# Kernel optimization log

Measured on AMD Instinct MI355X. Metric: run time of the kernel, lower is better.

The kernel has to match this reference:

```python
import jax, jax.numpy as jnp
import numpy as np

B, N, F_IN, D = 4, 2048, 32, 64  # D = output_dim; gat1: heads=4, d=D//2=32; gat2: heads=1, d=D


def _gat(x, adj_norm, Wq, bq, Wk, bk, Wv, bv, heads, d):
    b, n, _ = x.shape
    q = (x @ Wq + bq).reshape(b, n, heads, d)
    k = (x @ Wk + bk).reshape(b, n, heads, d)
    v = (x @ Wv + bv).reshape(b, n, heads, d)
    scores = jnp.einsum('bihd,bjhd->bhij', q, k) / jnp.sqrt(jnp.float32(d))
    mask = jnp.where(adj_norm == 0, jnp.float32(-1e9), jnp.float32(0.0))  # [N,N]
    w = jax.nn.softmax(scores + mask[None, None], axis=-1)
    out = jnp.einsum('bhij,bjhd->bihd', w, v)
    return out.reshape(b, n, heads * d)


def setup_inputs() -> dict:
    key = jax.random.key(0)
    ks = jax.random.split(key, 12)
    s = 0.05
    x = jax.random.normal(ks[0], (B, N, F_IN), dtype=jnp.float32)
    adj = (jax.random.uniform(ks[1], (N, N)) < 0.02).astype(jnp.float32)  # sparse binary graph
    return {
        'x': x, 'adj': adj,
        'Wp': jax.random.normal(ks[2], (F_IN, D)) * s, 'bp': jnp.zeros((D,), jnp.float32),
        'Wq1': jax.random.normal(ks[3], (F_IN, 2 * D)) * s, 'bq1': jnp.zeros((2 * D,), jnp.float32),
        'Wk1': jax.random.normal(ks[4], (F_IN, 2 * D)) * s, 'bk1': jnp.zeros((2 * D,), jnp.float32),
        'Wv1': jax.random.normal(ks[5], (F_IN, 2 * D)) * s, 'bv1': jnp.zeros((2 * D,), jnp.float32),
        'Wq2': jax.random.normal(ks[6], (2 * D, D)) * s, 'bq2': jnp.zeros((D,), jnp.float32),
        'Wk2': jax.random.normal(ks[7], (2 * D, D)) * s, 'bk2': jnp.zeros((D,), jnp.float32),
        'Wv2': jax.random.normal(ks[8], (2 * D, D)) * s, 'bv2': jnp.zeros((D,), jnp.float32),
        'gamma': jnp.ones((D,), jnp.float32), 'beta': jnp.zeros((D,), jnp.float32),
    }


def reference(x, adj, Wp, bp, Wq1, bq1, Wk1, bk1, Wv1, bv1,
              Wq2, bq2, Wk2, bk2, Wv2, bv2, gamma, beta):
    # row-normalized adjacency (normalize_adjacency)
    adj_n = adj / (jnp.sum(adj, axis=1, keepdims=True) + 1e-6)
    proj = x @ Wp + bp                                   # [B,N,D]
    h = _gat(x, adj_n, Wq1, bq1, Wk1, bk1, Wv1, bv1, 4, D // 2)   # [B,N,2D]
    h = jax.nn.relu(h)                                   # dropout inactive (training=False)
    h = _gat(h, adj_n, Wq2, bq2, Wk2, bk2, Wv2, bv2, 1, D)        # [B,N,D]
    y = h + proj
    mu = jnp.mean(y, axis=-1, keepdims=True)
    var = jnp.var(y, axis=-1, keepdims=True)
    return gamma * (y - mu) / jnp.sqrt(var + 1e-6) + beta
```

## Files before the change

### kernel.cpp

```cpp
#include <hip/hip_runtime.h>
#include <hip/hip_bf16.h>
#include <hip/hip_fp16.h>

#define BB 4
#define NN 2048
#define FIN 32
#define DD 64
#define MAXDEG 128

__device__ __forceinline__ __half2 u2h2(unsigned u) {
    union { unsigned u; __half2 h; } x; x.u = u; return x.h;
}

__global__ __launch_bounds__(128) void csr_gemm1(const float* __restrict__ adj,
    int* __restrict__ deg, int* __restrict__ col,
    const float* __restrict__ x,
    const float* __restrict__ Wp, const float* __restrict__ bp,
    const float* __restrict__ Wq, const float* __restrict__ bq,
    const float* __restrict__ Wk, const float* __restrict__ bk,
    const float* __restrict__ Wv, const float* __restrict__ bv,
    float* __restrict__ proj, __half* __restrict__ q1,
    __half* __restrict__ k1, __half* __restrict__ v1) {
    const int bid = blockIdx.x;
    const int tid = threadIdx.x;

    if (bid < NN / 2) {
        const int lane = tid & 63;
        const int i = bid * 2 + (tid >> 6);
        const unsigned long long below = (1ull << lane) - 1ull;
        int base = 0;
        for (int j0 = 0; j0 < NN; j0 += 256) {
            const float4 a = *(const float4*)(adj + (size_t)i * NN + j0 + lane * 4);
            const bool n0 = a.x != 0.0f, n1 = a.y != 0.0f, n2 = a.z != 0.0f, n3 = a.w != 0.0f;
            const unsigned long long m0 = __ballot(n0);
            const unsigned long long m1 = __ballot(n1);
            const unsigned long long m2 = __ballot(n2);
            const unsigned long long m3 = __ballot(n3);
            int slot = base + __popcll(m0 & below) + __popcll(m1 & below)
                            + __popcll(m2 & below) + __popcll(m3 & below);
            const int jb = j0 + 4 * lane;
            if (n0) { if (slot < MAXDEG) col[i * MAXDEG + slot] = jb;     ++slot; }
            if (n1) { if (slot < MAXDEG) col[i * MAXDEG + slot] = jb + 1; ++slot; }
            if (n2) { if (slot < MAXDEG) col[i * MAXDEG + slot] = jb + 2; ++slot; }
            if (n3) { if (slot < MAXDEG) col[i * MAXDEG + slot] = jb + 3; ++slot; }
            base += __popcll(m0) + __popcll(m1) + __popcll(m2) + __popcll(m3);
        }
        if (lane == 0) deg[i] = base < MAXDEG ? base : MAXDEG;
        return;
    }

    const int g = bid - NN / 2;
    const int b = g & 3;
    const int half = (g >> 2) & 1;
    const int w = g >> 3;
    const int r0 = b * NN + half * 1024 + w * 4;
    __shared__ float xs[FIN * 4];
    {
        const int r = tid >> 5, k = tid & 31;
        xs[k * 4 + r] = x[(size_t)r0 * FIN + tid];
    }
    __syncthreads();

    float aq0 = bq[tid], aq1 = aq0, aq2 = aq0, aq3 = aq0;
    float ak0 = bk[tid], ak1 = ak0, ak2 = ak0, ak3 = ak0;
    float av0 = bv[tid], av1 = av0, av2 = av0, av3 = av0;
    #pragma unroll
    for (int k = 0; k < FIN; ++k) {
        const float wq = Wq[k * 128 + tid];
        const float wk = Wk[k * 128 + tid];
        const float wv = Wv[k * 128 + tid];
        const float4 xv = *(const float4*)&xs[k * 4];
        aq0 = fmaf(xv.x, wq, aq0); aq1 = fmaf(xv.y, wq, aq1);
        aq2 = fmaf(xv.z, wq, aq2); aq3 = fmaf(xv.w, wq, aq3);
        ak0 = fmaf(xv.x, wk, ak0); ak1 = fmaf(xv.y, wk, ak1);
        ak2 = fmaf(xv.z, wk, ak2); ak3 = fmaf(xv.w, wk, ak3);
        av0 = fmaf(xv.x, wv, av0); av1 = fmaf(xv.y, wv, av1);
        av2 = fmaf(xv.z, wv, av2); av3 = fmaf(xv.w, wv, av3);
    }
    q1[(size_t)(r0 + 0) * 128 + tid] = __float2half_rn(aq0);
    q1[(size_t)(r0 + 1) * 128 + tid] = __float2half_rn(aq1);
    q1[(size_t)(r0 + 2) * 128 + tid] = __float2half_rn(aq2);
    q1[(size_t)(r0 + 3) * 128 + tid] = __float2half_rn(aq3);
    k1[(size_t)(r0 + 0) * 128 + tid] = __float2half_rn(ak0);
    k1[(size_t)(r0 + 1) * 128 + tid] = __float2half_rn(ak1);
    k1[(size_t)(r0 + 2) * 128 + tid] = __float2half_rn(ak2);
    k1[(size_t)(r0 + 3) * 128 + tid] = __float2half_rn(ak3);
    v1[(size_t)(r0 + 0) * 128 + tid] = __float2half_rn(av0);
    v1[(size_t)(r0 + 1) * 128 + tid] = __float2half_rn(av1);
    v1[(size_t)(r0 + 2) * 128 + tid] = __float2half_rn(av2);
    v1[(size_t)(r0 + 3) * 128 + tid] = __float2half_rn(av3);

    if (tid < 64) {
        float a0 = bp[tid], a1 = a0, a2 = a0, a3 = a0;
        #pragma unroll
        for (int k = 0; k < FIN; ++k) {
            const float wp = Wp[k * 64 + tid];
            const float4 xv = *(const float4*)&xs[k * 4];
            a0 = fmaf(xv.x, wp, a0); a1 = fmaf(xv.y, wp, a1);
            a2 = fmaf(xv.z, wp, a2); a3 = fmaf(xv.w, wp, a3);
        }
        proj[(size_t)(r0 + 0) * 64 + tid] = a0; proj[(size_t)(r0 + 1) * 64 + tid] = a1;
        proj[(size_t)(r0 + 2) * 64 + tid] = a2; proj[(size_t)(r0 + 3) * 64 + tid] = a3;
    }
}

__global__ __launch_bounds__(192) void gemm2_fused(const __half* __restrict__ h,
    const float* __restrict__ Wq, const float* __restrict__ bq,
    const float* __restrict__ Wk, const float* __restrict__ bk,
    const float* __restrict__ Wv, const float* __restrict__ bv,
    __half* __restrict__ q2, __half* __restrict__ k2, __half* __restrict__ v2) {
    const int bid = blockIdx.x;
    const int b = bid & 3;
    const int half = (bid >> 2) & 1;
    const int w = bid >> 3;
    const int r0 = b * NN + half * 1024 + w * 8;
    const int tid = threadIdx.x;
    const int mat = tid / 64;
    const int c = tid & 63;
    __shared__ float xs[128][8];
    for (int idx = tid; idx < 512; idx += 192) {
        const __half2 hv = ((const __half2*)(h + (size_t)r0 * 128))[idx];
        const int flat = idx * 2;
        const int r = flat >> 7, k = flat & 127;
        xs[k][r] = __low2float(hv); xs[k + 1][r] = __high2float(hv);
    }
    __syncthreads();

    const float* __restrict__ W   = mat == 0 ? Wq : (mat == 1 ? Wk : Wv);
    const float* __restrict__ bia = mat == 0 ? bq : (mat == 1 ? bk : bv);
    __half* __restrict__ Y        = mat == 0 ? q2 : (mat == 1 ? k2 : v2);

    float acc[8];
    const float b0 = bia[c];
    #pragma unroll
    for (int r = 0; r < 8; ++r) acc[r] = b0;
    #pragma unroll 4
    for (int k = 0; k < 128; ++k) {
        const float wv = W[(size_t)k * 64 + c];
        const float4 xa = *(const float4*)&xs[k][0];
        const float4 xb = *(const float4*)&xs[k][4];
        acc[0] = fmaf(xa.x, wv, acc[0]); acc[1] = fmaf(xa.y, wv, acc[1]);
        acc[2] = fmaf(xa.z, wv, acc[2]); acc[3] = fmaf(xa.w, wv, acc[3]);
        acc[4] = fmaf(xb.x, wv, acc[4]); acc[5] = fmaf(xb.y, wv, acc[5]);
        acc[6] = fmaf(xb.z, wv, acc[6]); acc[7] = fmaf(xb.w, wv, acc[7]);
    }
    #pragma unroll
    for (int r = 0; r < 8; ++r) Y[(size_t)(r0 + r) * 64 + c] = __float2half_rn(acc[r]);
}

__device__ __forceinline__ void map_bi4(int bid, int wid, int& b, int& i) {
    const int xcd = bid & 7;
    b = xcd & 3;
    i = ((xcd >> 2) << 10) | ((bid >> 3) << 2) | wid;
}

__global__ __launch_bounds__(256) void attn1_relu(const __half* __restrict__ q1,
                                                  const __half* __restrict__ k1,
                                                  const __half* __restrict__ v1,
                                                  const int* __restrict__ deg,
                                                  const int* __restrict__ col,
                                                  __half* __restrict__ h) {
    const int wid = threadIdx.x >> 6;
    const int lane = threadIdx.x & 63;
    int b, i;
    map_bi4(blockIdx.x, wid, b, i);

    __shared__ float wsA[4][4][MAXDEG + 8];
    const size_t stride = (size_t)NN * 128;
    const size_t bbase = (size_t)b * stride;
    const int d = deg[i];

    int jA = 0, jB = 0;
    if (lane < d) jA = col[i * MAXDEG + lane];
    if (64 + lane < d) jB = col[i * MAXDEG + 64 + lane];

    const int hh   = lane >> 4;
    const int t    = lane & 15;
    const int nbr8 = t & 7;
    const int e    = t >> 3;

    __half2 qh[8];
    {
        const __half* qbase = q1 + bbase + (size_t)i * 128 + hh * 32 + e * 16;
        const uint4 qa = *(const uint4*)qbase;
        const uint4 qb = *(const uint4*)(qbase + 8);
        qh[0] = u2h2(qa.x); qh[1] = u2h2(qa.y); qh[2] = u2h2(qa.z); qh[3] = u2h2(qa.w);
        qh[4] = u2h2(qb.x); qh[5] = u2h2(qb.y); qh[6] = u2h2(qb.z); qh[7] = u2h2(qb.w);
    }

    const float scale = 0.17677669529663687f;
    float sc[16];
    #pragma unroll
    for (int r = 0; r < 16; ++r) sc[r] = -INFINITY;

    #pragma unroll
    for (int r = 0; r < 16; ++r) {
        if (r * 8 < d) {
            const int slot = r * 8 + nbr8;
            const int jx = __shfl(jA, slot & 63);
            const int jy = __shfl(jB, slot & 63);
            const int j = (slot < 64) ? jx : jy;
            float p = 0.0f;
            if (slot < d) {
                const __half* kr = k1 + bbase + (size_t)j * 128 + hh * 32 + e * 16;
                const uint4 ka = *(const uint4*)kr;
                const uint4 kb = *(const uint4*)(kr + 8);
                __half2 a2 = __float2half2_rn(0.0f), b2 = __float2half2_rn(0.0f);
                a2 = __hfma2(qh[0], u2h2(ka.x), a2); b2 = __hfma2(qh[1], u2h2(ka.y), b2);
                a2 = __hfma2(qh[2], u2h2(ka.z), a2); b2 = __hfma2(qh[3], u2h2(ka.w), b2);
                a2 = __hfma2(qh[4], u2h2(kb.x), a2); b2 = __hfma2(qh[5], u2h2(kb.y), b2);
                a2 = __hfma2(qh[6], u2h2(kb.z), a2); b2 = __hfma2(qh[7], u2h2(kb.w), b2);
                p = (__low2float(a2) + __high2float(a2)) +
                    (__low2float(b2) + __high2float(b2));
            }
            p += __shfl_xor(p, 8);
            if (slot < d) sc[r] = p * scale;
        }
    }

    float mx = -INFINITY;
    #pragma unroll
    for (int r = 0; r < 16; ++r) mx = fmaxf(mx, sc[r]);
    #pragma unroll
    for (int off = 8; off >= 1; off >>= 1) mx = fmaxf(mx, __shfl_xor(mx, off));
    float se = 0.0f;
    #pragma unroll
    for (int r = 0; r < 16; ++r) {
        if (r * 8 < d) {
            const float ex = __expf(sc[r] - mx);
            sc[r] = ex;
            se += ex;
        }
    }
    #pragma unroll
    for (int off = 8; off >= 1; off >>= 1) se += __shfl_xor(se, off);
    const float inv = (d > 0) ? 2.0f / se : 0.0f;
    if (e == 0) {
        #pragma unroll
        for (int r = 0; r < 16; ++r) {
            if (r * 8 < d) {
                const int slot = r * 8 + nbr8;
                if (slot < d) wsA[wid][hh][slot] = sc[r] * inv;
            }
        }
    }
    asm volatile("s_waitcnt lgkmcnt(0)" ::: "memory");

    const float* __restrict__ wp = wsA[wid][lane >> 4];
    const int4* __restrict__ cp4 = (const int4*)(col + i * MAXDEG);
    const __half* __restrict__ vrow = v1 + bbase + 2 * lane;
    float a0 = 0.0f, a1 = 0.0f, b0 = 0.0f, b1 = 0.0f;
    float c0 = 0.0f, c1 = 0.0f, e0 = 0.0f, e1 = 0.0f;
    int t2 = 0;
    for (; t2 + 4 <= d; t2 += 4) {
        const int4 j4 = cp4[t2 >> 2];
        const float w0 = wp[t2], w1 = wp[t2 + 1], w2 = wp[t2 + 2], w3 = wp[t2 + 3];
        const __half2 v0 = u2h2(*(const unsigned*)(vrow + (size_t)j4.x * 128));
        const __half2 v1h = u2h2(*(const unsigned*)(vrow + (size_t)j4.y * 128));
        const __half2 v2h = u2h2(*(const unsigned*)(vrow + (size_t)j4.z * 128));
        const __half2 v3h = u2h2(*(const unsigned*)(vrow + (size_t)j4.w * 128));
        a0 = fmaf(w0, __low2float(v0), a0);  a1 = fmaf(w0, __high2float(v0), a1);
        b0 = fmaf(w1, __low2float(v1h), b0); b1 = fmaf(w1, __high2float(v1h), b1);
        c0 = fmaf(w2, __low2float(v2h), c0); c1 = fmaf(w2, __high2float(v2h), c1);
        e0 = fmaf(w3, __low2float(v3h), e0); e1 = fmaf(w3, __high2float(v3h), e1);
    }
    for (; t2 < d; ++t2) {
        const int j = col[i * MAXDEG + t2];
        const float w0 = wp[t2];
        const __half2 v0 = u2h2(*(const unsigned*)(vrow + (size_t)j * 128));
        a0 = fmaf(w0, __low2float(v0), a0);  a1 = fmaf(w0, __high2float(v0), a1);
    }
    float o0 = (a0 + b0) + (c0 + e0);
    float o1 = (a1 + b1) + (c1 + e1);
    if (d == 0) {
        float s0 = 0.0f, s1 = 0.0f;
        for (int j = 0; j < NN; ++j) {
            const __half2 vj = u2h2(*(const unsigned*)(vrow + (size_t)j * 128));
            s0 += __low2float(vj); s1 += __high2float(vj);
        }
        o0 = s0 * (1.0f / NN); o1 = s1 * (1.0f / NN);
    }
    o0 = fmaxf(o0, 0.0f); o1 = fmaxf(o1, 0.0f);
    ((__half2*)(h + bbase + (size_t)i * 128))[lane] =
        __halves2half2(__float2half_rn(o0), __float2half_rn(o1));
}

__global__ __launch_bounds__(256) void attn2_ln(const __half* __restrict__ q2,
                                                const __half* __restrict__ k2,
                                                const __half* __restrict__ v2,
                                                const float* __restrict__ proj,
                                                const int* __restrict__ deg,
                                                const int* __restrict__ col,
                                                const float* __restrict__ gamma,
                                                const float* __restrict__ beta,
                                                float* __restrict__ out) {
    const int wid = threadIdx.x >> 6;
    const int lane = threadIdx.x & 63;
    int b, i;
    map_bi4(blockIdx.x, wid, b, i);

    __shared__ float ws2[4][MAXDEG];
    __shared__ float att_lds[4][64];
    const size_t stride = (size_t)NN * 64;
    const size_t bbase = (size_t)b * stride;
    const int d = deg[i];

    int jA = 0, jB = 0;
    if (lane < d) jA = col[i * MAXDEG + lane];
    if (64 + lane < d) jB = col[i * MAXDEG + 64 + lane];

    const int g = lane >> 3;
    const int e = lane & 7;

    __half2 qh[4];
    {
        const uint4 qa = *(const uint4*)(q2 + bbase + (size_t)i * 64 + e * 8);
        qh[0] = u2h2(qa.x); qh[1] = u2h2(qa.y); qh[2] = u2h2(qa.z); qh[3] = u2h2(qa.w);
    }

    const float scale = 0.125f;
    float sc[16];
    #pragma unroll
    for (int r = 0; r < 16; ++r) sc[r] = -INFINITY;

    #pragma unroll
    for (int r = 0; r < 16; ++r) {
        if (r * 8 < d) {
            const int slot = r * 8 + g;
            const int jx = __shfl(jA, slot & 63);
            const int jy = __shfl(jB, slot & 63);
            const int j = (slot < 64) ? jx : jy;
            float p = 0.0f;
            if (slot < d) {
                const uint4 ka = *(const uint4*)(k2 + bbase + (size_t)j * 64 + e * 8);
                __half2 a2 = __float2half2_rn(0.0f), b2 = __float2half2_rn(0.0f);
                a2 = __hfma2(qh[0], u2h2(ka.x), a2); b2 = __hfma2(qh[1], u2h2(ka.y), b2);
                a2 = __hfma2(qh[2], u2h2(ka.z), a2); b2 = __hfma2(qh[3], u2h2(ka.w), b2);
                p = (__low2float(a2) + __high2float(a2)) +
                    (__low2float(b2) + __high2float(b2));
            }
            p += __shfl_xor(p, 1);
            p += __shfl_xor(p, 2);
            p += __shfl_xor(p, 4);
            if (slot < d) sc[r] = p * scale;
        }
    }

    float mx = -INFINITY;
    #pragma unroll
    for (int r = 0; r < 16; ++r) mx = fmaxf(mx, sc[r]);
    #pragma unroll
    for (int off = 32; off >= 1; off >>= 1) mx = fmaxf(mx, __shfl_xor(mx, off));
    float se = 0.0f;
    #pragma unroll
    for (int r = 0; r < 16; ++r) {
        if (r * 8 < d) {
            const float ex = __expf(sc[r] - mx);
            sc[r] = ex;
            se += ex;
        }
    }
    #pragma unroll
    for (int off = 32; off >= 1; off >>= 1) se += __shfl_xor(se, off);
    const float inv = (d > 0) ? 8.0f / se : 0.0f;
    if (e == 0) {
        #pragma unroll
        for (int r = 0; r < 16; ++r) {
            if (r * 8 < d) {
                const int slot = r * 8 + g;
                if (slot < d) ws2[wid][slot] = sc[r] * inv;
            }
        }
    }
    asm volatile("s_waitcnt lgkmcnt(0)" ::: "memory");

    const int p = lane & 31, g2 = lane >> 5;
    const float* __restrict__ wp = ws2[wid];
    const __half* __restrict__ vrow = v2 + bbase + 2 * p;
    float a0 = 0.0f, a1 = 0.0f, b0 = 0.0f, b1 = 0.0f;
    int t2 = g2;
    for (; t2 + 2 < d; t2 += 4) {
        const int ja = col[i * MAXDEG + t2], jb = col[i * MAXDEG + t2 + 2];
        const __half2 va = u2h2(*(const unsigned*)(vrow + (size_t)ja * 64));
        const __half2 vb = u2h2(*(const unsigned*)(vrow + (size_t)jb * 64));
        const float wa = wp[t2], wb = wp[t2 + 2];
        a0 = fmaf(wa, __low2float(va), a0); a1 = fmaf(wa, __high2float(va), a1);
        b0 = fmaf(wb, __low2float(vb), b0); b1 = fmaf(wb, __high2float(vb), b1);
    }
    if (t2 < d) {
        const int ja = col[i * MAXDEG + t2];
        const __half2 va = u2h2(*(const unsigned*)(vrow + (size_t)ja * 64));
        const float wa = wp[t2];
        a0 = fmaf(wa, __low2float(va), a0); a1 = fmaf(wa, __high2float(va), a1);
    }
    a0 += b0; a1 += b1;
    a0 += __shfl_xor(a0, 32);
    a1 += __shfl_xor(a1, 32);
    if (g2 == 0) { att_lds[wid][2 * p] = a0; att_lds[wid][2 * p + 1] = a1; }
    asm volatile("s_waitcnt lgkmcnt(0)" ::: "memory");
    float att = att_lds[wid][lane];
    if (d == 0) {
        float a = 0.0f;
        const __half* vr = v2 + bbase + lane;
        for (int j = 0; j < NN; ++j) a += __half2float(vr[(size_t)j * 64]);
        att = a * (1.0f / NN);
    }

    const float y = att + proj[bbase + (size_t)i * 64 + lane];
    float s = y;
    s += __shfl_xor(s, 32); s += __shfl_xor(s, 16); s += __shfl_xor(s, 8);
    s += __shfl_xor(s, 4);  s += __shfl_xor(s, 2);  s += __shfl_xor(s, 1);
    const float mu = s * (1.0f / 64.0f);
    const float yc = y - mu;
    float sq = yc * yc;
    sq += __shfl_xor(sq, 32); sq += __shfl_xor(sq, 16); sq += __shfl_xor(sq, 8);
    sq += __shfl_xor(sq, 4);  sq += __shfl_xor(sq, 2);  sq += __shfl_xor(sq, 1);
    const float var = sq * (1.0f / 64.0f);
    out[bbase + (size_t)i * 64 + lane] =
        gamma[lane] * yc * rsqrtf(var + 1e-6f) + beta[lane];
}

extern "C" void kernel_launch(void* const* d_in, const int* in_sizes, int n_in,
                              void* d_out, int out_size, void* d_ws, size_t ws_size,
                              hipStream_t stream) {
    const float* x     = (const float*)d_in[0];
    const float* adj   = (const float*)d_in[1];
    const float* Wp    = (const float*)d_in[2];
    const float* bp    = (const float*)d_in[3];
    const float* Wq1   = (const float*)d_in[4];
    const float* bq1   = (const float*)d_in[5];
    const float* Wk1   = (const float*)d_in[6];
    const float* bk1   = (const float*)d_in[7];
    const float* Wv1   = (const float*)d_in[8];
    const float* bv1   = (const float*)d_in[9];
    const float* Wq2   = (const float*)d_in[10];
    const float* bq2   = (const float*)d_in[11];
    const float* Wk2   = (const float*)d_in[12];
    const float* bk2   = (const float*)d_in[13];
    const float* Wv2   = (const float*)d_in[14];
    const float* bv2   = (const float*)d_in[15];
    const float* gamma = (const float*)d_in[16];
    const float* beta  = (const float*)d_in[17];
    float* out = (float*)d_out;

    char* ws = (char*)d_ws;
    size_t off = 0;
    auto alloc = [&](size_t bytes) {
        void* p = ws + off;
        off = (off + bytes + 255) & ~(size_t)255;
        return p;
    };
    int*    deg  = (int*)   alloc((size_t)NN * 4);
    int*    col  = (int*)   alloc((size_t)NN * MAXDEG * 4);
    float*  proj = (float*) alloc((size_t)BB * NN * 64 * 4);
    __half* q1   = (__half*)alloc((size_t)BB * NN * 128 * 2);
    __half* k1   = (__half*)alloc((size_t)BB * NN * 128 * 2);
    __half* v1   = (__half*)alloc((size_t)BB * NN * 128 * 2);
    __half* h    = (__half*)alloc((size_t)BB * NN * 128 * 2);
    __half* q2   = (__half*)alloc((size_t)BB * NN * 64 * 2);
    __half* k2   = (__half*)alloc((size_t)BB * NN * 64 * 2);
    __half* v2   = (__half*)alloc((size_t)BB * NN * 64 * 2);

    csr_gemm1<<<NN / 2 + BB * NN / 4, 128, 0, stream>>>(
        adj, deg, col, x, Wp, bp, Wq1, bq1, Wk1, bk1, Wv1, bv1, proj, q1, k1, v1);

    attn1_relu<<<BB * NN / 4, 256, 0, stream>>>(q1, k1, v1, deg, col, h);

    gemm2_fused<<<BB * NN / 8, 192, 0, stream>>>(h, Wq2, bq2, Wk2, bk2, Wv2, bv2,
                                                 q2, k2, v2);

    attn2_ln<<<BB * NN / 4, 256, 0, stream>>>(q2, k2, v2, proj, deg, col, gamma, beta, out);
}
```

Before: 62.95 us.

## Fuse second-layer QKV projection into first attention kernel via shared memory

```diff
diff --git a/kernel.cpp b/kernel.cpp
--- a/kernel.cpp
+++ b/kernel.cpp
@@ -5,22 +5,24 @@
 #define BB 4
 #define NN 2048
 #define FIN 32
-#define DD 64
 #define MAXDEG 128
 
 __device__ __forceinline__ __half2 u2h2(unsigned u) {
     union { unsigned u; __half2 h; } x; x.u = u; return x.h;
 }
 
-__global__ __launch_bounds__(128) void csr_gemm1(const float* __restrict__ adj,
+__global__ __launch_bounds__(128) void csr_gemm1w(const float* __restrict__ adj,
     int* __restrict__ deg, int* __restrict__ col,
     const float* __restrict__ x,
     const float* __restrict__ Wp, const float* __restrict__ bp,
     const float* __restrict__ Wq, const float* __restrict__ bq,
     const float* __restrict__ Wk, const float* __restrict__ bk,
     const float* __restrict__ Wv, const float* __restrict__ bv,
+    const float* __restrict__ Wq2, const float* __restrict__ Wk2,
+    const float* __restrict__ Wv2,
     float* __restrict__ proj, __half* __restrict__ q1,
-    __half* __restrict__ k1, __half* __restrict__ v1) {
+    __half* __restrict__ k1, __half* __restrict__ v1,
+    __half* __restrict__ Wh) {
     const int bid = blockIdx.x;
     const int tid = threadIdx.x;
 
@@ -48,12 +50,17 @@
         if (lane == 0) deg[i] = base < MAXDEG ? base : MAXDEG;
         return;
     }
-
-    const int g = bid - NN / 2;
-    const int b = g & 3;
-    const int half = (g >> 2) & 1;
-    const int w = g >> 3;
-    const int r0 = b * NN + half * 1024 + w * 4;
+    if (bid >= NN / 2 + 2048) {
+        const int t0 = (bid - NN / 2 - 2048) * 128 + tid;
+        for (int e2 = t0; e2 < 3 * 8192; e2 += 256) {
+            const int mat = e2 >> 13, idx = e2 & 8191;
+            const float* src = mat == 0 ? Wq2 : (mat == 1 ? Wk2 : Wv2);
+            Wh[e2] = __float2half_rn(src[idx]);
+        }
+        return;
+    }
+
+    const int r0 = (bid - NN / 2) * 4;
     __shared__ float xs[FIN * 4];
     {
         const int r = tid >> 5, k = tid & 31;
@@ -104,68 +111,26 @@
     }
 }
 
-__global__ __launch_bounds__(192) void gemm2_fused(const __half* __restrict__ h,
-    const float* __restrict__ Wq, const float* __restrict__ bq,
-    const float* __restrict__ Wk, const float* __restrict__ bk,
-    const float* __restrict__ Wv, const float* __restrict__ bv,
-    __half* __restrict__ q2, __half* __restrict__ k2, __half* __restrict__ v2) {
-    const int bid = blockIdx.x;
-    const int b = bid & 3;
-    const int half = (bid >> 2) & 1;
-    const int w = bid >> 3;
-    const int r0 = b * NN + half * 1024 + w * 8;
-    const int tid = threadIdx.x;
-    const int mat = tid / 64;
-    const int c = tid & 63;
-    __shared__ float xs[128][8];
-    for (int idx = tid; idx < 512; idx += 192) {
-        const __half2 hv = ((const __half2*)(h + (size_t)r0 * 128))[idx];
-        const int flat = idx * 2;
-        const int r = flat >> 7, k = flat & 127;
-        xs[k][r] = __low2float(hv); xs[k + 1][r] = __high2float(hv);
-    }
-    __syncthreads();
-
-    const float* __restrict__ W   = mat == 0 ? Wq : (mat == 1 ? Wk : Wv);
-    const float* __restrict__ bia = mat == 0 ? bq : (mat == 1 ? bk : bv);
-    __half* __restrict__ Y        = mat == 0 ? q2 : (mat == 1 ? k2 : v2);
-
-    float acc[8];
-    const float b0 = bia[c];
-    #pragma unroll
-    for (int r = 0; r < 8; ++r) acc[r] = b0;
-    #pragma unroll 4
-    for (int k = 0; k < 128; ++k) {
-        const float wv = W[(size_t)k * 64 + c];
-        const float4 xa = *(const float4*)&xs[k][0];
-        const float4 xb = *(const float4*)&xs[k][4];
-        acc[0] = fmaf(xa.x, wv, acc[0]); acc[1] = fmaf(xa.y, wv, acc[1]);
-        acc[2] = fmaf(xa.z, wv, acc[2]); acc[3] = fmaf(xa.w, wv, acc[3]);
-        acc[4] = fmaf(xb.x, wv, acc[4]); acc[5] = fmaf(xb.y, wv, acc[5]);
-        acc[6] = fmaf(xb.z, wv, acc[6]); acc[7] = fmaf(xb.w, wv, acc[7]);
-    }
-    #pragma unroll
-    for (int r = 0; r < 8; ++r) Y[(size_t)(r0 + r) * 64 + c] = __float2half_rn(acc[r]);
-}
-
-__device__ __forceinline__ void map_bi4(int bid, int wid, int& b, int& i) {
-    const int xcd = bid & 7;
-    b = xcd & 3;
-    i = ((xcd >> 2) << 10) | ((bid >> 3) << 2) | wid;
-}
-
-__global__ __launch_bounds__(256) void attn1_relu(const __half* __restrict__ q1,
-                                                  const __half* __restrict__ k1,
-                                                  const __half* __restrict__ v1,
-                                                  const int* __restrict__ deg,
-                                                  const int* __restrict__ col,
-                                                  __half* __restrict__ h) {
+__global__ __launch_bounds__(256) void attn1_gemm2(const __half* __restrict__ q1,
+                                                   const __half* __restrict__ k1,
+                                                   const __half* __restrict__ v1,
+                                                   const int* __restrict__ deg,
+                                                   const int* __restrict__ col,
+                                                   const __half* __restrict__ Wh,
+                                                   const float* __restrict__ bq2,
+                                                   const float* __restrict__ bk2,
+                                                   const float* __restrict__ bv2,
+                                                   __half* __restrict__ q2,
+                                                   __half* __restrict__ k2,
+                                                   __half* __restrict__ v2) {
     const int wid = threadIdx.x >> 6;
     const int lane = threadIdx.x & 63;
-    int b, i;
-    map_bi4(blockIdx.x, wid, b, i);
+    const int b = blockIdx.x >> 9;
+    const int i0 = (blockIdx.x & 511) * 4;
+    const int i = i0 + wid;
 
     __shared__ float wsA[4][4][MAXDEG + 8];
+    __shared__ __half hs[4][128];
     const size_t stride = (size_t)NN * 128;
     const size_t bbase = (size_t)b * stride;
     const int d = deg[i];
@@ -281,8 +246,38 @@
         o0 = s0 * (1.0f / NN); o1 = s1 * (1.0f / NN);
     }
     o0 = fmaxf(o0, 0.0f); o1 = fmaxf(o1, 0.0f);
-    ((__half2*)(h + bbase + (size_t)i * 128))[lane] =
+    ((__half2*)&hs[wid][0])[lane] =
         __halves2half2(__float2half_rn(o0), __float2half_rn(o1));
+    __syncthreads();
+
+    const int mat = threadIdx.x >> 6;
+    if (mat < 3) {
+        const int c = lane;
+        const float* bia = mat == 0 ? bq2 : (mat == 1 ? bk2 : bv2);
+        const __half* __restrict__ Wm = Wh + mat * 8192 + c;
+        const float bb0 = bia[c];
+        float acc0 = bb0, acc1 = bb0, acc2 = bb0, acc3 = bb0;
+        #pragma unroll 8
+        for (int k = 0; k < 128; ++k) {
+            const float wv = __half2float(Wm[k * 64]);
+            acc0 = fmaf(wv, __half2float(hs[0][k]), acc0);
+            acc1 = fmaf(wv, __half2float(hs[1][k]), acc1);
+            acc2 = fmaf(wv, __half2float(hs[2][k]), acc2);
+            acc3 = fmaf(wv, __half2float(hs[3][k]), acc3);
+        }
+        __half* __restrict__ Y = mat == 0 ? q2 : (mat == 1 ? k2 : v2);
+        const size_t rb = (size_t)b * NN + i0;
+        Y[(rb + 0) * 64 + c] = __float2half_rn(acc0);
+        Y[(rb + 1) * 64 + c] = __float2half_rn(acc1);
+        Y[(rb + 2) * 64 + c] = __float2half_rn(acc2);
+        Y[(rb + 3) * 64 + c] = __float2half_rn(acc3);
+    }
+}
+
+__device__ __forceinline__ void map_bi4(int bid, int wid, int& b, int& i) {
+    const int xcd = bid & 7;
+    b = xcd & 3;
+    i = ((xcd >> 2) << 10) | ((bid >> 3) << 2) | wid;
 }
 
 __global__ __launch_bounds__(256) void attn2_ln(const __half* __restrict__ q2,
@@ -456,18 +451,18 @@
     __half* q1   = (__half*)alloc((size_t)BB * NN * 128 * 2);
     __half* k1   = (__half*)alloc((size_t)BB * NN * 128 * 2);
     __half* v1   = (__half*)alloc((size_t)BB * NN * 128 * 2);
-    __half* h    = (__half*)alloc((size_t)BB * NN * 128 * 2);
     __half* q2   = (__half*)alloc((size_t)BB * NN * 64 * 2);
     __half* k2   = (__half*)alloc((size_t)BB * NN * 64 * 2);
     __half* v2   = (__half*)alloc((size_t)BB * NN * 64 * 2);
-
-    csr_gemm1<<<NN / 2 + BB * NN / 4, 128, 0, stream>>>(
-        adj, deg, col, x, Wp, bp, Wq1, bq1, Wk1, bk1, Wv1, bv1, proj, q1, k1, v1);
-
-    attn1_relu<<<BB * NN / 4, 256, 0, stream>>>(q1, k1, v1, deg, col, h);
-
-    gemm2_fused<<<BB * NN / 8, 192, 0, stream>>>(h, Wq2, bq2, Wk2, bk2, Wv2, bv2,
-                                                 q2, k2, v2);
-
-    attn2_ln<<<BB * NN / 4, 256, 0, stream>>>(q2, k2, v2, proj, deg, col, gamma, beta, out);
-}
+    __half* Wh   = (__half*)alloc((size_t)3 * 8192 * 2);
+
+    csr_gemm1w<<<NN / 2 + 2048 + 2, 128, 0, stream>>>(
+        adj, deg, col, x, Wp, bp, Wq1, bq1, Wk1, bk1, Wv1, bv1,
+        Wq2, Wk2, Wv2, proj, q1, k1, v1, Wh);
+
+    attn1_gemm2<<<2048, 256, 0, stream>>>(q1, k1, v1, deg, col, Wh,
+                                          bq2, bk2, bv2, q2, k2, v2);
+
+    attn2_ln<<<2048, 256, 0, stream>>>(q2, k2, v2, proj, deg, col,
+                                       gamma, beta, out);
+}
```

Result: slower. 70.96 us (+12.7%).
